# Optimization experiments

Hardware: AMD Instinct MI355X
Metric: run time of the kernel (lower is better)

The kernel has to match this reference:

```python
import jax, jax.numpy as jnp
import numpy as np

B, E, H, NF, NO, L = 1024, 256, 4, 16384, 49152, 192
DH = E // H
NEG = -1e9  # effectively -inf for masked-out padded keys


def _positions(batch, n, offset_counts=None):
    # batch is sorted; within-segment index = i - segment_start[batch[i]]
    counts = jax.ops.segment_sum(jnp.ones((n,), jnp.int32), batch, num_segments=B)
    start = jnp.cumsum(counts) - counts
    pos = jnp.arange(n, dtype=jnp.int32) - start[batch]
    if offset_counts is not None:
        pos = pos + offset_counts[batch]
    return pos, counts


def setup_inputs() -> dict:
    key = jax.random.key(0)
    ks = jax.random.split(key, 8)
    scene_feat = jax.random.normal(ks[0], (B, E), jnp.float32)
    face_nodes = jax.random.normal(ks[1], (NF, E), jnp.float32)
    obj_nodes = jax.random.normal(ks[2], (NO, E), jnp.float32)
    face_batch = jnp.sort(jax.random.randint(ks[3], (NF,), 0, B))
    obj_batch = jnp.sort(jax.random.randint(ks[4], (NO,), 0, B))
    s = 1.0 / np.sqrt(E)
    in_proj_w = jax.random.uniform(ks[5], (3 * E, E), jnp.float32, -s, s)
    in_proj_b = jnp.zeros((3 * E,), jnp.float32)
    out_proj_w = jax.random.uniform(ks[6], (E, E), jnp.float32, -s, s)
    out_proj_b = jnp.zeros((E,), jnp.float32)
    ln_gamma = jnp.ones((E,), jnp.float32)
    ln_beta = jnp.zeros((E,), jnp.float32)
    return dict(scene_feat=scene_feat, face_nodes=face_nodes, obj_nodes=obj_nodes,
                face_batch=face_batch, obj_batch=obj_batch,
                in_proj_w=in_proj_w, in_proj_b=in_proj_b,
                out_proj_w=out_proj_w, out_proj_b=out_proj_b,
                ln_gamma=ln_gamma, ln_beta=ln_beta)


def reference(scene_feat, face_nodes, obj_nodes, face_batch, obj_batch,
              in_proj_w, in_proj_b, out_proj_w, out_proj_b, ln_gamma, ln_beta):
    # --- to_dense_batch over concat([face, obj]) : faces first per graph ---
    pos_f, counts_f = _positions(face_batch, NF)
    pos_o, _ = _positions(obj_batch, NO, offset_counts=counts_f)
    all_nodes = jnp.concatenate([face_nodes, obj_nodes], axis=0)   # [N, E]
    all_batch = jnp.concatenate([face_batch, obj_batch], axis=0)   # [N]
    all_pos = jnp.concatenate([pos_f, pos_o], axis=0)              # [N]
    slot = jnp.where(all_pos < L, all_pos, L)                      # overflow -> sentinel col
    dense = jnp.zeros((B, L + 1, E), all_nodes.dtype).at[all_batch, slot].set(all_nodes)[:, :L]
    mask = jnp.zeros((B, L + 1), bool).at[all_batch, slot].set(True)[:, :L]

    # --- single-query multihead cross-attention (torch MHA semantics) ---
    wq, wk, wv = in_proj_w[:E], in_proj_w[E:2 * E], in_proj_w[2 * E:]
    bq, bk, bv = in_proj_b[:E], in_proj_b[E:2 * E], in_proj_b[2 * E:]
    q = (scene_feat @ wq.T + bq).reshape(B, H, DH)                 # [B,H,DH]
    k = (dense @ wk.T + bk).reshape(B, L, H, DH)
    v = (dense @ wv.T + bv).reshape(B, L, H, DH)
    scores = jnp.einsum('bhd,blhd->bhl', q, k) / np.sqrt(DH)        # [B,H,L]
    scores = jnp.where(mask[:, None, :], scores, NEG)
    attn = jax.nn.softmax(scores, axis=-1)                          # [B,H,L]
    ctx = jnp.einsum('bhl,blhd->bhd', attn, v).reshape(B, E)
    attn_out = ctx @ out_proj_w.T + out_proj_b                      # [B,E]

    # --- residual + LayerNorm ---
    x = scene_feat + attn_out
    mu = jnp.mean(x, axis=-1, keepdims=True)
    var = jnp.mean(jnp.square(x - mu), axis=-1, keepdims=True)
    fused = (x - mu) * jax.lax.rsqrt(var + 1e-5) * ln_gamma + ln_beta  # [B,E]

    attn_weights = jnp.mean(attn, axis=1)[:, None, :]               # [B,1,L] head-averaged
    return fused, attn_weights
```

## Files before the change

kernel.cpp:

```cpp
#include <hip/hip_runtime.h>
#include <math.h>

#define B 1024
#define E 256
#define H 4
#define DH 64
#define L 192
#define NF 16384
#define NO 49152
#define BPB 4

__global__ __launch_bounds__(256) void prep_kernel(
    const int* __restrict__ fb, const int* __restrict__ ob,
    int* __restrict__ start_f, int* __restrict__ start_o,
    const float* __restrict__ ipw, const float* __restrict__ opw,
    float* __restrict__ WT)
{
  int blk = blockIdx.x;
  if (blk < 192) {
    int m = blk / 64;
    int r = blk % 64;
    int bx = (r & 7) * 32, by = (r >> 3) * 32;
    const float* src = (m == 0) ? ipw : (m == 1 ? ipw + 2 * E * E : opw);
    float* dst = WT + (size_t)m * E * E;
    __shared__ float tile[32][33];
    int tx = threadIdx.x & 31, ty = threadIdx.x >> 5;
#pragma unroll
    for (int i = 0; i < 32; i += 8)
      tile[ty + i][tx] = src[(size_t)(by + ty + i) * E + bx + tx];
    __syncthreads();
#pragma unroll
    for (int i = 0; i < 32; i += 8)
      dst[(size_t)(bx + ty + i) * E + by + tx] = tile[tx][ty + i];
  } else {
    int b = (blk - 192) * 256 + threadIdx.x;
    if (b > B) return;
    int lo = 0, hi = NF;
    while (lo < hi) { int m = (lo + hi) >> 1; if (fb[m] < b) lo = m + 1; else hi = m; }
    start_f[b] = lo;
    lo = 0; hi = NO;
    while (lo < hi) { int m = (lo + hi) >> 1; if (ob[m] < b) lo = m + 1; else hi = m; }
    start_o[b] = lo;
  }
}

__global__ __launch_bounds__(512, 2) void fused_kernel(
    const float* __restrict__ scene,
    const float* __restrict__ face, const float* __restrict__ obj,
    const float* __restrict__ ipw, const float* __restrict__ ipb,
    const float* __restrict__ WqT, const float* __restrict__ WvT,
    const float* __restrict__ WoT, const float* __restrict__ opb,
    const float* __restrict__ gamma, const float* __restrict__ beta,
    const int* __restrict__ start_f, const int* __restrict__ start_o,
    float* __restrict__ fusedO, float* __restrict__ attnw)
{
  int b0 = blockIdx.x * BPB;
  int t = threadIdx.x, wave = t >> 6, lane = t & 63;

  __shared__ float sc_s[BPB][E];
  __shared__ float q_s[BPB][E];
  __shared__ float YZ_s[BPB][H][E];
  __shared__ float ctx_s[BPB][E];
  __shared__ float s_s[BPB][H][L];
  __shared__ float un_s[8192];
  __shared__ float mw_s[BPB][2][2], su_s[BPB][2][2], sb_s[BPB][H];
  __shared__ int   info_s[BPB][4];

  for (int i = t; i < BPB * E; i += 512)
    ((float*)sc_s)[i] = scene[(size_t)b0 * E + i];
  if (t < BPB) {
    int b = b0 + t;
    int sf0 = start_f[b], cf = start_f[b + 1] - sf0;
    int so0 = start_o[b], co = start_o[b + 1] - so0;
    info_s[t][0] = sf0; info_s[t][1] = so0;
    info_s[t][2] = min(cf, L); info_s[t][3] = min(cf + co, L);
  }
  __syncthreads();

  {
    const float4* W4 = (const float4*)WqT + lane;
    float4 a0 = {0,0,0,0}, a1 = {0,0,0,0}, a2 = {0,0,0,0}, a3 = {0,0,0,0};
    int j0 = wave * 32;
#pragma unroll
    for (int jj = 0; jj < 32; ++jj) {
      int j = j0 + jj;
      float4 w = W4[(size_t)j * 64];
      float s0 = sc_s[0][j], s1 = sc_s[1][j], s2 = sc_s[2][j], s3 = sc_s[3][j];
      a0.x += s0*w.x; a0.y += s0*w.y; a0.z += s0*w.z; a0.w += s0*w.w;
      a1.x += s1*w.x; a1.y += s1*w.y; a1.z += s1*w.z; a1.w += s1*w.w;
      a2.x += s2*w.x; a2.y += s2*w.y; a2.z += s2*w.z; a2.w += s2*w.w;
      a3.x += s3*w.x; a3.y += s3*w.y; a3.z += s3*w.z; a3.w += s3*w.w;
    }
    *(float4*)&un_s[((wave * BPB + 0) << 8) + 4 * lane] = a0;
    *(float4*)&un_s[((wave * BPB + 1) << 8) + 4 * lane] = a1;
    *(float4*)&un_s[((wave * BPB + 2) << 8) + 4 * lane] = a2;
    *(float4*)&un_s[((wave * BPB + 3) << 8) + 4 * lane] = a3;
  }
  __syncthreads();
  for (int i = t; i < BPB * E; i += 512) {
    int bi = i >> 8, e = i & 255;
    float v = ipb[e];
#pragma unroll
    for (int w = 0; w < 8; ++w) v += un_s[((w * BPB + bi) << 8) + e];
    q_s[bi][e] = v;
  }
  __syncthreads();

  if (wave < BPB) {
#pragma unroll
    for (int h = 0; h < H; ++h) {
      float v = q_s[wave][h * DH + lane] * ipb[E + h * DH + lane];
#pragma unroll
      for (int o = 32; o; o >>= 1) v += __shfl_xor(v, o);
      if (lane == 0) sb_s[wave][h] = v;
    }
  }

  {
    const float* Wk = ipw + (size_t)E * E;
    int h = wave >> 1, d0 = (wave & 1) * 32, wi = wave & 1;
    float4 a0 = {0,0,0,0}, a1 = {0,0,0,0}, a2 = {0,0,0,0}, a3 = {0,0,0,0};
#pragma unroll
    for (int dd = 0; dd < 32; ++dd) {
      int d = d0 + dd;
      float4 w = *((const float4*)(Wk + (size_t)(h * DH + d) * E) + lane);
      float q0 = q_s[0][h * DH + d], q1 = q_s[1][h * DH + d];
      float q2 = q_s[2][h * DH + d], q3 = q_s[3][h * DH + d];
      a0.x += q0*w.x; a0.y += q0*w.y; a0.z += q0*w.z; a0.w += q0*w.w;
      a1.x += q1*w.x; a1.y += q1*w.y; a1.z += q1*w.z; a1.w += q1*w.w;
      a2.x += q2*w.x; a2.y += q2*w.y; a2.z += q2*w.z; a2.w += q2*w.w;
      a3.x += q3*w.x; a3.y += q3*w.y; a3.z += q3*w.z; a3.w += q3*w.w;
    }
    *(float4*)&un_s[wi * 4096 + ((0 * H + h) << 8) + 4 * lane] = a0;
    *(float4*)&un_s[wi * 4096 + ((1 * H + h) << 8) + 4 * lane] = a1;
    *(float4*)&un_s[wi * 4096 + ((2 * H + h) << 8) + 4 * lane] = a2;
    *(float4*)&un_s[wi * 4096 + ((3 * H + h) << 8) + 4 * lane] = a3;
  }
  __syncthreads();
  for (int i = t; i < BPB * H * E; i += 512)
    ((float*)YZ_s)[i] = un_s[i] + un_s[4096 + i];
  __syncthreads();

  {
    int bb = wave >> 1, hp = wave & 1, h0 = hp * 2;
    int g = lane >> 4, sl = lane & 15;
    int sf0 = info_s[bb][0], so0 = info_s[bb][1];
    int n_f = info_s[bb][2], n = info_s[bb][3];

    float4 y[2][4];
#pragma unroll
    for (int hh = 0; hh < 2; ++hh)
#pragma unroll
      for (int k = 0; k < 4; ++k)
        y[hh][k] = *(const float4*)&YZ_s[bb][h0 + hh][4 * (sl + 16 * k)];
    float sbv[2] = {sb_s[bb][h0], sb_s[bb][h0 + 1]};

    float m[2] = {-3.0e38f, -3.0e38f};
    float u[2] = {0.f, 0.f};
    float4 acc[2][4] = {};

    float4 x[4] = {};
    if (g < n) {
      const float* xr = (g < n_f) ? face + (size_t)(sf0 + g) * E
                                  : obj  + (size_t)(so0 + g - n_f) * E;
#pragma unroll
      for (int k = 0; k < 4; ++k) x[k] = ((const float4*)xr)[sl + 16 * k];
    }

    for (int s = g; s < n; s += 4) {
      float4 xn[4] = {};
      int sn = s + 4;
      if (sn < n) {
        const float* xr = (sn < n_f) ? face + (size_t)(sf0 + sn) * E
                                     : obj  + (size_t)(so0 + sn - n_f) * E;
#pragma unroll
        for (int k = 0; k < 4; ++k) xn[k] = ((const float4*)xr)[sl + 16 * k];
      }

      float p[2];
#pragma unroll
      for (int hh = 0; hh < 2; ++hh) {
        float a = 0.f;
#pragma unroll
        for (int k = 0; k < 4; ++k)
          a += x[k].x * y[hh][k].x + x[k].y * y[hh][k].y +
               x[k].z * y[hh][k].z + x[k].w * y[hh][k].w;
        p[hh] = a;
      }
#pragma unroll
      for (int off = 8; off; off >>= 1) {
        p[0] += __shfl_xor(p[0], off);
        p[1] += __shfl_xor(p[1], off);
      }
      p[0] = (p[0] + sbv[0]) * 0.125f;
      p[1] = (p[1] + sbv[1]) * 0.125f;
      if (sl == 0) {
        s_s[bb][h0][s] = p[0];
        s_s[bb][h0 + 1][s] = p[1];
      }
#pragma unroll
      for (int hh = 0; hh < 2; ++hh) {
        if (p[hh] > m[hh]) {
          float f = __expf(m[hh] - p[hh]);
#pragma unroll
          for (int k = 0; k < 4; ++k) {
            acc[hh][k].x = acc[hh][k].x * f + x[k].x;
            acc[hh][k].y = acc[hh][k].y * f + x[k].y;
            acc[hh][k].z = acc[hh][k].z * f + x[k].z;
            acc[hh][k].w = acc[hh][k].w * f + x[k].w;
          }
          u[hh] = u[hh] * f + 1.f;
          m[hh] = p[hh];
        } else {
          float e = __expf(p[hh] - m[hh]);
#pragma unroll
          for (int k = 0; k < 4; ++k) {
            acc[hh][k].x += e * x[k].x;
            acc[hh][k].y += e * x[k].y;
            acc[hh][k].z += e * x[k].z;
            acc[hh][k].w += e * x[k].w;
          }
          u[hh] += e;
        }
      }
#pragma unroll
      for (int k = 0; k < 4; ++k) x[k] = xn[k];
    }

#pragma unroll
    for (int off = 16; off <= 32; off <<= 1) {
#pragma unroll
      for (int hh = 0; hh < 2; ++hh) {
        float mo = __shfl_xor(m[hh], off);
        float uo = __shfl_xor(u[hh], off);
        float M = fmaxf(m[hh], mo);
        float fs = __expf(m[hh] - M), fo = __expf(mo - M);
        u[hh] = fs * u[hh] + fo * uo;
        m[hh] = M;
#pragma unroll
        for (int k = 0; k < 4; ++k) {
          float ax = __shfl_xor(acc[hh][k].x, off);
          float ay = __shfl_xor(acc[hh][k].y, off);
          float az = __shfl_xor(acc[hh][k].z, off);
          float aw = __shfl_xor(acc[hh][k].w, off);
          acc[hh][k].x = fs * acc[hh][k].x + fo * ax;
          acc[hh][k].y = fs * acc[hh][k].y + fo * ay;
          acc[hh][k].z = fs * acc[hh][k].z + fo * az;
          acc[hh][k].w = fs * acc[hh][k].w + fo * aw;
        }
      }
    }
    if (g == 0) {
#pragma unroll
      for (int hh = 0; hh < 2; ++hh)
#pragma unroll
        for (int k = 0; k < 4; ++k)
          *(float4*)&un_s[(((bb * 2 + hp) * 2 + hh) << 8) + 4 * (sl + 16 * k)] = acc[hh][k];
    }
    if (lane == 0) {
      mw_s[bb][hp][0] = m[0]; mw_s[bb][hp][1] = m[1];
      su_s[bb][hp][0] = u[0]; su_s[bb][hp][1] = u[1];
    }
  }
  __syncthreads();

  for (int i = t; i < BPB * H * E; i += 512) {
    int bi = i >> 10, rem = i & 1023, h = rem >> 8, e = rem & 255;
    float z = 0.f;
    if (info_s[bi][3] > 0) {
      int hp = h >> 1, hh = h & 1;
      float inv = 1.0f / su_s[bi][hp][hh];
      z = un_s[(((bi * 2 + hp) * 2 + hh) << 8) + e] * inv;
    }
    ((float*)YZ_s)[i] = z;
  }
  for (int i = t; i < BPB * L; i += 512) {
    int bi = i / L, s = i - bi * L;
    int n = info_s[bi][3];
    float v;
    if (n == 0) v = 1.0f / L;
    else if (s < n) {
      v = 0.f;
#pragma unroll
      for (int h = 0; h < H; ++h) {
        int hp = h >> 1, hh = h & 1;
        v += __expf(s_s[bi][h][s] - mw_s[bi][hp][hh]) / su_s[bi][hp][hh];
      }
      v *= 0.25f;
    } else v = 0.f;
    attnw[(size_t)(b0 + bi) * L + s] = v;
  }
  __syncthreads();

  {
    const float4* W4 = (const float4*)WvT + lane;
    int j0 = wave * 32, hoff = (lane >> 4) * E;
    float4 a0 = {0,0,0,0}, a1 = {0,0,0,0}, a2 = {0,0,0,0}, a3 = {0,0,0,0};
#pragma unroll
    for (int jj = 0; jj < 32; ++jj) {
      int j = j0 + jj;
      float4 w = W4[(size_t)j * 64];
      float z0 = ((float*)YZ_s[0])[hoff + j];
      float z1 = ((float*)YZ_s[1])[hoff + j];
      float z2 = ((float*)YZ_s[2])[hoff + j];
      float z3 = ((float*)YZ_s[3])[hoff + j];
      a0.x += z0*w.x; a0.y += z0*w.y; a0.z += z0*w.z; a0.w += z0*w.w;
      a1.x += z1*w.x; a1.y += z1*w.y; a1.z += z1*w.z; a1.w += z1*w.w;
      a2.x += z2*w.x; a2.y += z2*w.y; a2.z += z2*w.z; a2.w += z2*w.w;
      a3.x += z3*w.x; a3.y += z3*w.y; a3.z += z3*w.z; a3.w += z3*w.w;
    }
    *(float4*)&un_s[((wave * BPB + 0) << 8) + 4 * lane] = a0;
    *(float4*)&un_s[((wave * BPB + 1) << 8) + 4 * lane] = a1;
    *(float4*)&un_s[((wave * BPB + 2) << 8) + 4 * lane] = a2;
    *(float4*)&un_s[((wave * BPB + 3) << 8) + 4 * lane] = a3;
  }
  __syncthreads();
  for (int i = t; i < BPB * E; i += 512) {
    int bi = i >> 8, e = i & 255;
    float v = ipb[2 * E + e];
#pragma unroll
    for (int w = 0; w < 8; ++w) v += un_s[((w * BPB + bi) << 8) + e];
    ctx_s[bi][e] = v;
  }
  __syncthreads();

  {
    const float4* W4 = (const float4*)WoT + lane;
    int j0 = wave * 32;
    float4 a0 = {0,0,0,0}, a1 = {0,0,0,0}, a2 = {0,0,0,0}, a3 = {0,0,0,0};
#pragma unroll
    for (int jj = 0; jj < 32; ++jj) {
      int j = j0 + jj;
      float4 w = W4[(size_t)j * 64];
      float c0 = ctx_s[0][j], c1 = ctx_s[1][j], c2 = ctx_s[2][j], c3 = ctx_s[3][j];
      a0.x += c0*w.x; a0.y += c0*w.y; a0.z += c0*w.z; a0.w += c0*w.w;
      a1.x += c1*w.x; a1.y += c1*w.y; a1.z += c1*w.z; a1.w += c1*w.w;
      a2.x += c2*w.x; a2.y += c2*w.y; a2.z += c2*w.z; a2.w += c2*w.w;
      a3.x += c3*w.x; a3.y += c3*w.y; a3.z += c3*w.z; a3.w += c3*w.w;
    }
    *(float4*)&un_s[((wave * BPB + 0) << 8) + 4 * lane] = a0;
    *(float4*)&un_s[((wave * BPB + 1) << 8) + 4 * lane] = a1;
    *(float4*)&un_s[((wave * BPB + 2) << 8) + 4 * lane] = a2;
    *(float4*)&un_s[((wave * BPB + 3) << 8) + 4 * lane] = a3;
  }
  __syncthreads();
  for (int i = t; i < BPB * E; i += 512) {
    int bi = i >> 8, e = i & 255;
    float v = opb[e] + sc_s[bi][e];
#pragma unroll
    for (int w = 0; w < 8; ++w) v += un_s[((w * BPB + bi) << 8) + e];
    q_s[bi][e] = v;
  }
  __syncthreads();

  if (wave < BPB) {
    float v0 = q_s[wave][lane], v1 = q_s[wave][lane + 64],
          v2 = q_s[wave][lane + 128], v3 = q_s[wave][lane + 192];
    float s1 = v0 + v1 + v2 + v3;
#pragma unroll
    for (int o = 32; o; o >>= 1) s1 += __shfl_xor(s1, o);
    float mu = s1 * (1.0f / E);
    float d0 = v0 - mu, d1 = v1 - mu, d2 = v2 - mu, d3 = v3 - mu;
    float s2 = d0*d0 + d1*d1 + d2*d2 + d3*d3;
#pragma unroll
    for (int o = 32; o; o >>= 1) s2 += __shfl_xor(s2, o);
    float inv = 1.0f / sqrtf(s2 * (1.0f / E) + 1e-5f);
    size_t base = (size_t)(b0 + wave) * E;
    fusedO[base + lane      ] = d0 * inv * gamma[lane      ] + beta[lane      ];
    fusedO[base + lane +  64] = d1 * inv * gamma[lane +  64] + beta[lane +  64];
    fusedO[base + lane + 128] = d2 * inv * gamma[lane + 128] + beta[lane + 128];
    fusedO[base + lane + 192] = d3 * inv * gamma[lane + 192] + beta[lane + 192];
  }
}

extern "C" void kernel_launch(void* const* d_in, const int* in_sizes, int n_in,
                              void* d_out, int out_size, void* d_ws, size_t ws_size,
                              hipStream_t stream) {
  const float* scene = (const float*)d_in[0];
  const float* face  = (const float*)d_in[1];
  const float* obj   = (const float*)d_in[2];
  const int*   fb    = (const int*)d_in[3];
  const int*   ob    = (const int*)d_in[4];
  const float* ipw   = (const float*)d_in[5];
  const float* ipb   = (const float*)d_in[6];
  const float* opw   = (const float*)d_in[7];
  const float* opb   = (const float*)d_in[8];
  const float* gam   = (const float*)d_in[9];
  const float* bet   = (const float*)d_in[10];

  float* fused = (float*)d_out;
  float* attnw = fused + (size_t)B * E;

  int* start_f = (int*)d_ws;
  int* start_o = start_f + (B + 1);
  float* WT   = (float*)((char*)d_ws + (16 << 10));
  float* WqT = WT;
  float* WvT = WT + (size_t)E * E;
  float* WoT = WT + (size_t)2 * E * E;

  prep_kernel<<<197, 256, 0, stream>>>(fb, ob, start_f, start_o, ipw, opw, WT);
  fused_kernel<<<B / BPB, 512, 0, stream>>>(scene, face, obj, ipw, ipb,
                                            WqT, WvT, WoT, opb, gam, bet,
                                            start_f, start_o, fused, attnw);
}
```

Measured before the change: 51.01 us.

## Halve batches per block and split key rows across two waves

```diff
diff --git a/kernel.cpp b/kernel.cpp
--- a/kernel.cpp
+++ b/kernel.cpp
@@ -8,7 +8,7 @@
 #define L 192
 #define NF 16384
 #define NO 49152
-#define BPB 4
+#define BPB 2
 
 __global__ __launch_bounds__(256) void prep_kernel(
     const int* __restrict__ fb, const int* __restrict__ ob,
@@ -62,12 +62,11 @@
   __shared__ float YZ_s[BPB][H][E];
   __shared__ float ctx_s[BPB][E];
   __shared__ float s_s[BPB][H][L];
-  __shared__ float un_s[8192];
-  __shared__ float mw_s[BPB][2][2], su_s[BPB][2][2], sb_s[BPB][H];
+  __shared__ float un_s[4096];
+  __shared__ float mw_s[BPB][2][2][2], su_s[BPB][2][2][2], sb_s[BPB][H];
   __shared__ int   info_s[BPB][4];
 
-  for (int i = t; i < BPB * E; i += 512)
-    ((float*)sc_s)[i] = scene[(size_t)b0 * E + i];
+  sc_s[t >> 8][t & 255] = scene[(size_t)b0 * E + t];
   if (t < BPB) {
     int b = b0 + t;
     int sf0 = start_f[b], cf = start_f[b + 1] - sf0;
@@ -79,26 +78,22 @@
 
   {
     const float4* W4 = (const float4*)WqT + lane;
-    float4 a0 = {0,0,0,0}, a1 = {0,0,0,0}, a2 = {0,0,0,0}, a3 = {0,0,0,0};
+    float4 a0 = {0,0,0,0}, a1 = {0,0,0,0};
     int j0 = wave * 32;
 #pragma unroll
     for (int jj = 0; jj < 32; ++jj) {
       int j = j0 + jj;
       float4 w = W4[(size_t)j * 64];
-      float s0 = sc_s[0][j], s1 = sc_s[1][j], s2 = sc_s[2][j], s3 = sc_s[3][j];
+      float s0 = sc_s[0][j], s1 = sc_s[1][j];
       a0.x += s0*w.x; a0.y += s0*w.y; a0.z += s0*w.z; a0.w += s0*w.w;
       a1.x += s1*w.x; a1.y += s1*w.y; a1.z += s1*w.z; a1.w += s1*w.w;
-      a2.x += s2*w.x; a2.y += s2*w.y; a2.z += s2*w.z; a2.w += s2*w.w;
-      a3.x += s3*w.x; a3.y += s3*w.y; a3.z += s3*w.z; a3.w += s3*w.w;
     }
     *(float4*)&un_s[((wave * BPB + 0) << 8) + 4 * lane] = a0;
     *(float4*)&un_s[((wave * BPB + 1) << 8) + 4 * lane] = a1;
-    *(float4*)&un_s[((wave * BPB + 2) << 8) + 4 * lane] = a2;
-    *(float4*)&un_s[((wave * BPB + 3) << 8) + 4 * lane] = a3;
-  }
-  __syncthreads();
-  for (int i = t; i < BPB * E; i += 512) {
-    int bi = i >> 8, e = i & 255;
+  }
+  __syncthreads();
+  {
+    int bi = t >> 8, e = t & 255;
     float v = ipb[e];
 #pragma unroll
     for (int w = 0; w < 8; ++w) v += un_s[((w * BPB + bi) << 8) + e];
@@ -119,30 +114,25 @@
   {
     const float* Wk = ipw + (size_t)E * E;
     int h = wave >> 1, d0 = (wave & 1) * 32, wi = wave & 1;
-    float4 a0 = {0,0,0,0}, a1 = {0,0,0,0}, a2 = {0,0,0,0}, a3 = {0,0,0,0};
+    float4 a0 = {0,0,0,0}, a1 = {0,0,0,0};
 #pragma unroll
     for (int dd = 0; dd < 32; ++dd) {
       int d = d0 + dd;
       float4 w = *((const float4*)(Wk + (size_t)(h * DH + d) * E) + lane);
       float q0 = q_s[0][h * DH + d], q1 = q_s[1][h * DH + d];
-      float q2 = q_s[2][h * DH + d], q3 = q_s[3][h * DH + d];
       a0.x += q0*w.x; a0.y += q0*w.y; a0.z += q0*w.z; a0.w += q0*w.w;
       a1.x += q1*w.x; a1.y += q1*w.y; a1.z += q1*w.z; a1.w += q1*w.w;
-      a2.x += q2*w.x; a2.y += q2*w.y; a2.z += q2*w.z; a2.w += q2*w.w;
-      a3.x += q3*w.x; a3.y += q3*w.y; a3.z += q3*w.z; a3.w += q3*w.w;
-    }
-    *(float4*)&un_s[wi * 4096 + ((0 * H + h) << 8) + 4 * lane] = a0;
-    *(float4*)&un_s[wi * 4096 + ((1 * H + h) << 8) + 4 * lane] = a1;
-    *(float4*)&un_s[wi * 4096 + ((2 * H + h) << 8) + 4 * lane] = a2;
-    *(float4*)&un_s[wi * 4096 + ((3 * H + h) << 8) + 4 * lane] = a3;
+    }
+    *(float4*)&un_s[wi * 2048 + ((0 * H + h) << 8) + 4 * lane] = a0;
+    *(float4*)&un_s[wi * 2048 + ((1 * H + h) << 8) + 4 * lane] = a1;
   }
   __syncthreads();
   for (int i = t; i < BPB * H * E; i += 512)
-    ((float*)YZ_s)[i] = un_s[i] + un_s[4096 + i];
-  __syncthreads();
-
-  {
-    int bb = wave >> 1, hp = wave & 1, h0 = hp * 2;
+    ((float*)YZ_s)[i] = un_s[i] + un_s[2048 + i];
+  __syncthreads();
+
+  {
+    int bb = wave >> 2, hp = (wave >> 1) & 1, rs = wave & 1, h0 = hp * 2;
     int g = lane >> 4, sl = lane & 15;
     int sf0 = info_s[bb][0], so0 = info_s[bb][1];
     int n_f = info_s[bb][2], n = info_s[bb][3];
@@ -159,17 +149,18 @@
     float u[2] = {0.f, 0.f};
     float4 acc[2][4] = {};
 
+    int s0 = rs * 4 + g;
     float4 x[4] = {};
-    if (g < n) {
-      const float* xr = (g < n_f) ? face + (size_t)(sf0 + g) * E
-                                  : obj  + (size_t)(so0 + g - n_f) * E;
+    if (s0 < n) {
+      const float* xr = (s0 < n_f) ? face + (size_t)(sf0 + s0) * E
+                                   : obj  + (size_t)(so0 + s0 - n_f) * E;
 #pragma unroll
       for (int k = 0; k < 4; ++k) x[k] = ((const float4*)xr)[sl + 16 * k];
     }
 
-    for (int s = g; s < n; s += 4) {
+    for (int s = s0; s < n; s += 8) {
       float4 xn[4] = {};
-      int sn = s + 4;
+      int sn = s + 8;
       if (sn < n) {
         const float* xr = (sn < n_f) ? face + (size_t)(sf0 + sn) * E
                                      : obj  + (size_t)(so0 + sn - n_f) * E;
@@ -255,11 +246,11 @@
       for (int hh = 0; hh < 2; ++hh)
 #pragma unroll
         for (int k = 0; k < 4; ++k)
-          *(float4*)&un_s[(((bb * 2 + hp) * 2 + hh) << 8) + 4 * (sl + 16 * k)] = acc[hh][k];
+          *(float4*)&un_s[((((bb * 2 + hp) * 2 + rs) * 2 + hh) << 8) + 4 * (sl + 16 * k)] = acc[hh][k];
     }
     if (lane == 0) {
-      mw_s[bb][hp][0] = m[0]; mw_s[bb][hp][1] = m[1];
-      su_s[bb][hp][0] = u[0]; su_s[bb][hp][1] = u[1];
+      mw_s[bb][hp][rs][0] = m[0]; mw_s[bb][hp][rs][1] = m[1];
+      su_s[bb][hp][rs][0] = u[0]; su_s[bb][hp][rs][1] = u[1];
     }
   }
   __syncthreads();
@@ -269,13 +260,17 @@
     float z = 0.f;
     if (info_s[bi][3] > 0) {
       int hp = h >> 1, hh = h & 1;
-      float inv = 1.0f / su_s[bi][hp][hh];
-      z = un_s[(((bi * 2 + hp) * 2 + hh) << 8) + e] * inv;
+      float ma = mw_s[bi][hp][0][hh], mb = mw_s[bi][hp][1][hh];
+      float M = fmaxf(ma, mb);
+      float fa = __expf(ma - M), fb = __expf(mb - M);
+      float inv = 1.0f / (fa * su_s[bi][hp][0][hh] + fb * su_s[bi][hp][1][hh]);
+      z = (fa * un_s[((((bi * 2 + hp) * 2 + 0) * 2 + hh) << 8) + e] +
+           fb * un_s[((((bi * 2 + hp) * 2 + 1) * 2 + hh) << 8) + e]) * inv;
     }
     ((float*)YZ_s)[i] = z;
   }
-  for (int i = t; i < BPB * L; i += 512) {
-    int bi = i / L, s = i - bi * L;
+  if (t < BPB * L) {
+    int bi = t / L, s = t - bi * L;
     int n = info_s[bi][3];
     float v;
     if (n == 0) v = 1.0f / L;
@@ -284,7 +279,11 @@
 #pragma unroll
       for (int h = 0; h < H; ++h) {
         int hp = h >> 1, hh = h & 1;
-        v += __expf(s_s[bi][h][s] - mw_s[bi][hp][hh]) / su_s[bi][hp][hh];
+        float ma = mw_s[bi][hp][0][hh], mb = mw_s[bi][hp][1][hh];
+        float M = fmaxf(ma, mb);
+        float fa = __expf(ma - M), fb = __expf(mb - M);
+        float inv = 1.0f / (fa * su_s[bi][hp][0][hh] + fb * su_s[bi][hp][1][hh]);
+        v += __expf(s_s[bi][h][s] - M) * inv;
       }
       v *= 0.25f;
     } else v = 0.f;
@@ -295,28 +294,22 @@
   {
     const float4* W4 = (const float4*)WvT + lane;
     int j0 = wave * 32, hoff = (lane >> 4) * E;
-    float4 a0 = {0,0,0,0}, a1 = {0,0,0,0}, a2 = {0,0,0,0}, a3 = {0,0,0,0};
+    float4 a0 = {0,0,0,0}, a1 = {0,0,0,0};
 #pragma unroll
     for (int jj = 0; jj < 32; ++jj) {
       int j = j0 + jj;
       float4 w = W4[(size_t)j * 64];
       float z0 = ((float*)YZ_s[0])[hoff + j];
       float z1 = ((float*)YZ_s[1])[hoff + j];
-      float z2 = ((float*)YZ_s[2])[hoff + j];
-      float z3 = ((float*)YZ_s[3])[hoff + j];
       a0.x += z0*w.x; a0.y += z0*w.y; a0.z += z0*w.z; a0.w += z0*w.w;
       a1.x += z1*w.x; a1.y += z1*w.y; a1.z += z1*w.z; a1.w += z1*w.w;
-      a2.x += z2*w.x; a2.y += z2*w.y; a2.z += z2*w.z; a2.w += z2*w.w;
-      a3.x += z3*w.x; a3.y += z3*w.y; a3.z += z3*w.z; a3.w += z3*w.w;
     }
     *(float4*)&un_s[((wave * BPB + 0) << 8) + 4 * lane] = a0;
     *(float4*)&un_s[((wave * BPB + 1) << 8) + 4 * lane] = a1;
-    *(float4*)&un_s[((wave * BPB + 2) << 8) + 4 * lane] = a2;
-    *(float4*)&un_s[((wave * BPB + 3) << 8) + 4 * lane] = a3;
-  }
-  __syncthreads();
-  for (int i = t; i < BPB * E; i += 512) {
-    int bi = i >> 8, e = i & 255;
+  }
+  __syncthreads();
+  {
+    int bi = t >> 8, e = t & 255;
     float v = ipb[2 * E + e];
 #pragma unroll
     for (int w = 0; w < 8; ++w) v += un_s[((w * BPB + bi) << 8) + e];
@@ -327,25 +320,21 @@
   {
     const float4* W4 = (const float4*)WoT + lane;
     int j0 = wave * 32;
-    float4 a0 = {0,0,0,0}, a1 = {0,0,0,0}, a2 = {0,0,0,0}, a3 = {0,0,0,0};
+    float4 a0 = {0,0,0,0}, a1 = {0,0,0,0};
 #pragma unroll
     for (int jj = 0; jj < 32; ++jj) {
       int j = j0 + jj;
       float4 w = W4[(size_t)j * 64];
-      float c0 = ctx_s[0][j], c1 = ctx_s[1][j], c2 = ctx_s[2][j], c3 = ctx_s[3][j];
+      float c0 = ctx_s[0][j], c1 = ctx_s[1][j];
       a0.x += c0*w.x; a0.y += c0*w.y; a0.z += c0*w.z; a0.w += c0*w.w;
       a1.x += c1*w.x; a1.y += c1*w.y; a1.z += c1*w.z; a1.w += c1*w.w;
-      a2.x += c2*w.x; a2.y += c2*w.y; a2.z += c2*w.z; a2.w += c2*w.w;
-      a3.x += c3*w.x; a3.y += c3*w.y; a3.z += c3*w.z; a3.w += c3*w.w;
     }
     *(float4*)&un_s[((wave * BPB + 0) << 8) + 4 * lane] = a0;
     *(float4*)&un_s[((wave * BPB + 1) << 8) + 4 * lane] = a1;
-    *(float4*)&un_s[((wave * BPB + 2) << 8) + 4 * lane] = a2;
-    *(float4*)&un_s[((wave * BPB + 3) << 8) + 4 * lane] = a3;
-  }
-  __syncthreads();
-  for (int i = t; i < BPB * E; i += 512) {
-    int bi = i >> 8, e = i & 255;
+  }
+  __syncthreads();
+  {
+    int bi = t >> 8, e = t & 255;
     float v = opb[e] + sc_s[bi][e];
 #pragma unroll
     for (int w = 0; w < 8; ++w) v += un_s[((w * BPB + bi) << 8) + e];
```

Result: slower. 62.06 us (+21.7%).
